# Kernel optimization log

Hardware: AMD Instinct MI355X
Metric: run time of the kernel (lower is better)

Reference implementation:

```python
import jax, jax.numpy as jnp
import numpy as np

B, L, E, H = 2, 1024, 1024, 16
D = E // H  # head_dim = 64
EPS = 1e-6


def setup_inputs() -> dict:
    key = jax.random.key(0)
    ks = jax.random.split(key, 6)
    x = jax.random.normal(ks[0], (B, L, E), dtype=jnp.float32)
    qkv_w = jax.random.normal(ks[1], (E, 3 * E), dtype=jnp.float32) / np.sqrt(E)
    qkv_b = jnp.zeros((3 * E,), dtype=jnp.float32)
    out_w = jax.random.normal(ks[2], (E, E), dtype=jnp.float32) / np.sqrt(E)
    out_b = jnp.zeros((E,), dtype=jnp.float32)
    norm1_w = jnp.ones((E,), dtype=jnp.float32)
    norm2_w = jnp.ones((E,), dtype=jnp.float32)
    mlp_w1 = jax.random.normal(ks[3], (E, 4 * E), dtype=jnp.float32) / np.sqrt(E)
    mlp_b1 = jnp.zeros((4 * E,), dtype=jnp.float32)
    mlp_w2 = jax.random.normal(ks[4], (4 * E, E), dtype=jnp.float32) / np.sqrt(4 * E)
    mlp_b2 = jnp.zeros((E,), dtype=jnp.float32)
    return dict(x=x, qkv_w=qkv_w, qkv_b=qkv_b, out_w=out_w, out_b=out_b,
                norm1_w=norm1_w, norm2_w=norm2_w,
                mlp_w1=mlp_w1, mlp_b1=mlp_b1, mlp_w2=mlp_w2, mlp_b2=mlp_b2)


def rmsnorm(x, w, eps=1e-6):
    var = jnp.mean(jnp.square(x), axis=-1, keepdims=True)
    return x * jax.lax.rsqrt(var + eps) * w


def cosformer_attn(x, qkv_w, qkv_b, out_w, out_b):
    b, l, e = x.shape
    qkv = x @ qkv_w + qkv_b
    q, k, v = jnp.split(qkv, 3, axis=-1)
    # [B, H, L, D]
    q = q.reshape(b, l, H, D).transpose(0, 2, 1, 3)
    k = k.reshape(b, l, H, D).transpose(0, 2, 1, 3)
    v = v.reshape(b, l, H, D).transpose(0, 2, 1, 3)
    positions = jnp.arange(l, dtype=jnp.float32).reshape(1, 1, l, 1)
    cos_w = jnp.cos(jnp.pi / 2 * positions / l)
    sin_w = jnp.sin(jnp.pi / 2 * positions / l)
    q_prime = jax.nn.relu(q)
    k_prime = jax.nn.relu(k)
    q_cos, q_sin = q_prime * cos_w, q_prime * sin_w
    k_cos, k_sin = k_prime * cos_w, k_prime * sin_w
    # running KV state: cumsum over L of per-position outer products [B,H,L,D,D]
    kv_cos_cumsum = jnp.cumsum(jnp.einsum('bhld,bhle->bhlde', k_cos, v), axis=2)
    context_cos = jnp.einsum('bhld,bhlde->bhle', q_cos, kv_cos_cumsum)
    kv_sin_cumsum = jnp.cumsum(jnp.einsum('bhld,bhle->bhlde', k_sin, v), axis=2)
    context_sin = jnp.einsum('bhld,bhlde->bhle', q_sin, kv_sin_cumsum)
    context = context_cos + context_sin
    k_cos_cumsum = jnp.cumsum(k_cos, axis=2)
    k_sin_cumsum = jnp.cumsum(k_sin, axis=2)
    norm = (jnp.einsum('bhld,bhld->bhl', q_cos, k_cos_cumsum)
            + jnp.einsum('bhld,bhld->bhl', q_sin, k_sin_cumsum))
    output = context / (norm[..., None] + EPS)
    output = output.transpose(0, 2, 1, 3).reshape(b, l, e)
    return output @ out_w + out_b


def reference(x, qkv_w, qkv_b, out_w, out_b, norm1_w, norm2_w,
              mlp_w1, mlp_b1, mlp_w2, mlp_b2):
    # pre-norm transformer block with cosformer causal linear attention
    h = x + cosformer_attn(rmsnorm(x, norm1_w), qkv_w, qkv_b, out_w, out_b)
    m = rmsnorm(h, norm2_w)
    m = jax.nn.gelu(m @ mlp_w1 + mlp_b1) @ mlp_w2 + mlp_b2
    return h + m
```

## Files before the change

kernel.cpp:

```cpp
#include <hip/hip_runtime.h>

#define TB_L 1024
#define TB_E 1024

typedef __attribute__((ext_vector_type(8))) short bf16x8;
typedef __attribute__((ext_vector_type(8))) unsigned short u16x8;
typedef __attribute__((ext_vector_type(4))) float floatx4;

#define AS1(p) ((const __attribute__((address_space(1))) void*)(p))
#define AS3(p) ((__attribute__((address_space(3))) void*)(p))

static __device__ __forceinline__ unsigned short f2bf(float x) {
  union { float f; unsigned u; } c; c.f = x;
  unsigned r = c.u + 0x7fff + ((c.u >> 16) & 1);
  return (unsigned short)(r >> 16);
}
static __device__ __forceinline__ float gelu_f(float x) {
  const float c0 = 0.7978845608028654f;
  const float c1 = 0.044715f;
  float x3 = x * x * x;
  return 0.5f * x * (1.0f + tanhf(c0 * (x + c1 * x3)));
}

static __device__ __forceinline__ int swz(int row, int bytecol) {
  return row * 128 +
         ((((bytecol >> 4) ^ ((row + (row >> 3)) & 7)) << 4) | (bytecol & 15));
}

__global__ __launch_bounds__(256) void rms_kernel(const float* __restrict__ x,
                                                  const float* __restrict__ w,
                                                  unsigned short* __restrict__ out) {
  const int row = blockIdx.x;
  const int tid = threadIdx.x;
  const float4 v = *(const float4*)(x + (size_t)row * TB_E + tid * 4);
  float s = v.x * v.x + v.y * v.y + v.z * v.z + v.w * v.w;
#pragma unroll
  for (int off = 32; off > 0; off >>= 1) s += __shfl_down(s, off);
  __shared__ float red[4];
  if ((tid & 63) == 0) red[tid >> 6] = s;
  __syncthreads();
  const float tot = red[0] + red[1] + red[2] + red[3];
  const float scale = rsqrtf(tot * (1.0f / TB_E) + 1e-6f);
  const float4 wv = *(const float4*)(w + tid * 4);
  ushort4 o;
  o.x = f2bf(v.x * scale * wv.x);
  o.y = f2bf(v.y * scale * wv.y);
  o.z = f2bf(v.z * scale * wv.z);
  o.w = f2bf(v.w * scale * wv.w);
  *(ushort4*)(out + (size_t)row * TB_E + tid * 4) = o;
}

__global__ __launch_bounds__(256) void transpose_all(
    const float* __restrict__ s0, const float* __restrict__ s1,
    const float* __restrict__ s2, const float* __restrict__ s3,
    unsigned short* __restrict__ d0, unsigned short* __restrict__ d1,
    unsigned short* __restrict__ d2, unsigned short* __restrict__ d3) {
  const int id = blockIdx.x;
  const float* in; unsigned short* out; int K, N, lid;
  if (id < 768)       { in = s0; out = d0; K = 1024; N = 3072; lid = id; }
  else if (id < 1024) { in = s1; out = d1; K = 1024; N = 1024; lid = id - 768; }
  else if (id < 2048) { in = s2; out = d2; K = 1024; N = 4096; lid = id - 1024; }
  else                { in = s3; out = d3; K = 4096; N = 1024; lid = id - 2048; }
  const int nx = N >> 6;
  const int n0 = (lid % nx) * 64, k0 = (lid / nx) * 64;
  __shared__ float t[64][65];
  const int tid = threadIdx.x;
#pragma unroll
  for (int rep = 0; rep < 4; ++rep) {
    const int r = rep * 16 + (tid >> 4);
    const int c = (tid & 15) * 4;
    const float4 v = *(const float4*)(in + (size_t)(k0 + r) * N + n0 + c);
    t[r][c] = v.x; t[r][c + 1] = v.y; t[r][c + 2] = v.z; t[r][c + 3] = v.w;
  }
  __syncthreads();
#pragma unroll
  for (int rep = 0; rep < 4; ++rep) {
    const int n = rep * 16 + (tid >> 4);
    const int k = (tid & 15) * 4;
    ushort4 o;
    o.x = f2bf(t[k + 0][n]);
    o.y = f2bf(t[k + 1][n]);
    o.z = f2bf(t[k + 2][n]);
    o.w = f2bf(t[k + 3][n]);
    *(ushort4*)(out + (size_t)(n0 + n) * K + k0 + k) = o;
  }
}

template <int BM, int BN, int BK, int WM, int WN, int NTH, bool GELU>
__global__ __launch_bounds__(NTH) void gemm_bf16(
    const unsigned short* __restrict__ A, const unsigned short* __restrict__ Bt,
    const float* __restrict__ bias, const float* __restrict__ res,
    float* __restrict__ Cf, unsigned short* __restrict__ Cb,
    float* __restrict__ Cpart, int M, int N, int K, int Ksl) {
  constexpr int NW = NTH / 64;
  constexpr int KC = BK / 32;
  constexpr int WCOLS = BN / WN;
  constexpr int MT = WM / 16;
  constexpr int NT = WN / 16;
  constexpr int ACH = (BM / 16) * KC;
  constexpr int BCH = (BN / 16) * KC;
  static_assert((BM / WM) * (BN / WN) == NW, "wave grid");
  static_assert(ACH % NW == 0 && BCH % NW == 0, "chunks divisible by waves");
  __shared__ __align__(16) unsigned short As[2][BM * BK];
  __shared__ __align__(16) unsigned short Bs[2][BN * BK];
  const int tid = threadIdx.x;
  const int wid = tid >> 6, lane = tid & 63;

  constexpr int G = 4;
  const int nbx = gridDim.x;
  const int flat = blockIdx.y * nbx + blockIdx.x;
  const int grp = flat / (G * nbx), rem = flat % (G * nbx);
  const int m0 = (grp * G + rem % G) * BM;
  const int n0 = (rem / G) * BN;

  const int k_off = blockIdx.z * Ksl;
  const int mbase = (wid / WCOLS) * WM, nbase = (wid % WCOLS) * WN;

  floatx4 acc[MT][NT];
#pragma unroll
  for (int i = 0; i < MT; ++i)
#pragma unroll
    for (int j = 0; j < NT; ++j) {
      floatx4 z = {0.f, 0.f, 0.f, 0.f};
      acc[i][j] = z;
    }

  const int srow = lane >> 2;
  const int scol = (lane & 3) * 8;
  const unsigned short* Ag = A + (size_t)m0 * K + k_off;
  const unsigned short* Bg = Bt + (size_t)n0 * K + k_off;
  const int fr = (lane & 15);
  const int fk = (lane >> 4) * 16;

  auto stage = [&](int buf, int k0) {
#pragma unroll
    for (int j = 0; j < ACH / NW; ++j) {
      const int ch = j * NW + wid;
      const int strip = ch / KC, half = ch % KC;
      __builtin_amdgcn_global_load_lds(
          AS1(Ag + (size_t)(strip * 16 + srow) * K + k0 + half * 32 + scol),
          AS3((char*)&As[buf][0] + ch * 1024), 16, 0, 0);
    }
#pragma unroll
    for (int j = 0; j < BCH / NW; ++j) {
      const int ch = j * NW + wid;
      const int strip = ch / KC, half = ch % KC;
      __builtin_amdgcn_global_load_lds(
          AS1(Bg + (size_t)(strip * 16 + srow) * K + k0 + half * 32 + scol),
          AS3((char*)&Bs[buf][0] + ch * 1024), 16, 0, 0);
    }
  };

  stage(0, 0);
  const int nsteps = Ksl / BK;
  for (int s = 0; s < nsteps; ++s) {
    __syncthreads();
    const int cur = s & 1;
    if (s + 1 < nsteps) stage(cur ^ 1, (s + 1) * BK);
    const char* Ab = (const char*)&As[cur][0];
    const char* Bb = (const char*)&Bs[cur][0];
#pragma unroll
    for (int g = 0; g < KC; ++g) {
      bf16x8 af[MT], bfr[NT];
#pragma unroll
      for (int i = 0; i < MT; ++i)
        af[i] = *(const bf16x8*)(Ab + ((mbase / 16 + i) * KC + g) * 1024 +
                                 fr * 64 + fk);
#pragma unroll
      for (int j = 0; j < NT; ++j)
        bfr[j] = *(const bf16x8*)(Bb + ((nbase / 16 + j) * KC + g) * 1024 +
                                  fr * 64 + fk);
#pragma unroll
      for (int i = 0; i < MT; ++i)
#pragma unroll
        for (int j = 0; j < NT; ++j)
          acc[i][j] = __builtin_amdgcn_mfma_f32_16x16x32_bf16(af[i], bfr[j],
                                                              acc[i][j], 0, 0, 0);
    }
  }

  const int mr = (lane >> 4) * 4;
  const int nc = lane & 15;
  float* P = Cpart ? (Cpart + (size_t)blockIdx.z * M * N) : nullptr;
#pragma unroll
  for (int i = 0; i < MT; ++i)
#pragma unroll
    for (int j = 0; j < NT; ++j) {
      const int n = n0 + nbase + j * 16 + nc;
      const float bv = bias ? bias[n] : 0.f;
#pragma unroll
      for (int r = 0; r < 4; ++r) {
        const int m = m0 + mbase + i * 16 + mr + r;
        float v = acc[i][j][r] + bv;
        if (GELU) v = gelu_f(v);
        if (res) v += res[(size_t)m * N + n];
        if (P) P[(size_t)m * N + n] = v;
        if (Cf) Cf[(size_t)m * N + n] = v;
        if (Cb) Cb[(size_t)m * N + n] = f2bf(v);
      }
    }
}

__global__ __launch_bounds__(256) void reduce_out(const float* __restrict__ P,
                                                  const float* __restrict__ h,
                                                  const float* __restrict__ b2,
                                                  float* __restrict__ out) {
  const int idx = (blockIdx.x * 256 + threadIdx.x) * 4;
  const int n = idx & 1023;
  const float4 a = *(const float4*)(P + idx);
  const float4 b = *(const float4*)(P + 2097152 + idx);
  const float4 hh = *(const float4*)(h + idx);
  const float4 bb = *(const float4*)(b2 + n);
  float4 o;
  o.x = a.x + b.x + hh.x + bb.x;
  o.y = a.y + b.y + hh.y + bb.y;
  o.z = a.z + b.z + hh.z + bb.z;
  o.w = a.w + b.w + hh.w + bb.w;
  *(float4*)(out + idx) = o;
}

__global__ __launch_bounds__(256) void attn_mfma(const unsigned short* __restrict__ qkv,
                                                 unsigned short* __restrict__ out) {
  const int it = blockIdx.x;
  const int bh = blockIdx.y;
  const int b = bh >> 4, h = bh & 15;
  const int tid = threadIdx.x;
  const int w = tid >> 6, lane = tid & 63;
  const int qd = lane >> 4, ln = lane & 15;
  const int i0 = it * 64;
  __shared__ __align__(16) char sq[8192];
  __shared__ __align__(16) char sk[8192];
  __shared__ __align__(16) char svt[8192];
  __shared__ __align__(16) char ss[8192];
  const unsigned short* base = qkv + (size_t)b * (TB_L * 3072) + h * 64;
  const float PH = 1.5339807878856412e-3f;

#pragma unroll
  for (int p = 0; p < 2; ++p) {
    const int flat = p * 256 + tid;
    const int r = flat >> 3, c = flat & 7;
    u16x8 v = *(const u16x8*)(base + (size_t)(i0 + r) * 3072 + c * 8);
#pragma unroll
    for (int z = 0; z < 8; ++z) v[z] = (v[z] & 0x8000) ? (unsigned short)0 : v[z];
    *(u16x8*)(sq + swz(r, c * 16)) = v;
  }
  __syncthreads();

  bf16x8 aq[2];
#pragma unroll
  for (int ks = 0; ks < 2; ++ks)
    aq[ks] = *(const bf16x8*)(sq + swz(w * 16 + ln, ks * 64 + qd * 16));

  float ci[4], si[4];
#pragma unroll
  for (int r = 0; r < 4; ++r)
    __sincosf(PH * (float)(i0 + w * 16 + qd * 4 + r), &si[r], &ci[r]);

  floatx4 acc_o[4], acc_n;
  {
    floatx4 z = {0.f, 0.f, 0.f, 0.f};
#pragma unroll
    for (int nt = 0; nt < 4; ++nt) acc_o[nt] = z;
    acc_n = z;
  }
  bf16x8 ones;
#pragma unroll
  for (int z = 0; z < 8; ++z) ones[z] = (short)0x3F80;

  for (int jt = 0; jt <= it; ++jt) {
    const int j0 = jt * 64;
    __syncthreads();
#pragma unroll
    for (int p = 0; p < 2; ++p) {
      const int flat = p * 256 + tid;
      const int r = flat >> 3, c = flat & 7;
      u16x8 kv = *(const u16x8*)(base + (size_t)(j0 + r) * 3072 + 1024 + c * 8);
#pragma unroll
      for (int z = 0; z < 8; ++z) kv[z] = (kv[z] & 0x8000) ? (unsigned short)0 : kv[z];
      *(u16x8*)(sk + swz(r, c * 16)) = kv;
      u16x8 vv = *(const u16x8*)(base + (size_t)(j0 + r) * 3072 + 2048 + c * 8);
#pragma unroll
      for (int z = 0; z < 8; ++z)
        *(unsigned short*)(svt + swz(c * 8 + z, r * 2)) = (unsigned short)vv[z];
    }
    __syncthreads();

    floatx4 s_acc[4];
    {
      floatx4 z = {0.f, 0.f, 0.f, 0.f};
#pragma unroll
      for (int nt = 0; nt < 4; ++nt) s_acc[nt] = z;
    }
#pragma unroll
    for (int ks = 0; ks < 2; ++ks)
#pragma unroll
      for (int nt = 0; nt < 4; ++nt) {
        const bf16x8 bk = *(const bf16x8*)(sk + swz(nt * 16 + ln, ks * 64 + qd * 16));
        s_acc[nt] = __builtin_amdgcn_mfma_f32_16x16x32_bf16(aq[ks], bk, s_acc[nt], 0, 0, 0);
      }

    float cj[4], sj[4];
#pragma unroll
    for (int nt = 0; nt < 4; ++nt)
      __sincosf(PH * (float)(j0 + nt * 16 + ln), &sj[nt], &cj[nt]);
    const bool diag = (jt == it);
    const int li = w * 16 + qd * 4;
#pragma unroll
    for (int nt = 0; nt < 4; ++nt) {
      const int jl = nt * 16 + ln;
#pragma unroll
      for (int r = 0; r < 4; ++r) {
        float val = s_acc[nt][r] * (ci[r] * cj[nt] + si[r] * sj[nt]);
        if (diag && jl > li + r) val = 0.f;
        *(unsigned short*)(ss + swz(li + r, jl * 2)) = f2bf(val);
      }
    }

#pragma unroll
    for (int ks = 0; ks < 2; ++ks) {
      const bf16x8 as = *(const bf16x8*)(ss + swz(w * 16 + ln, ks * 64 + qd * 16));
#pragma unroll
      for (int nt = 0; nt < 4; ++nt) {
        const bf16x8 bv = *(const bf16x8*)(svt + swz(nt * 16 + ln, ks * 64 + qd * 16));
        acc_o[nt] = __builtin_amdgcn_mfma_f32_16x16x32_bf16(as, bv, acc_o[nt], 0, 0, 0);
      }
      acc_n = __builtin_amdgcn_mfma_f32_16x16x32_bf16(as, ones, acc_n, 0, 0, 0);
    }
  }

#pragma unroll
  for (int r = 0; r < 4; ++r) {
    const float inv = 1.0f / (acc_n[r] + 1e-6f);
    unsigned short* op =
        out + (size_t)(b * TB_L + i0 + w * 16 + qd * 4 + r) * TB_E + h * 64;
#pragma unroll
    for (int nt = 0; nt < 4; ++nt) op[nt * 16 + ln] = f2bf(acc_o[nt][r] * inv);
  }
}

extern "C" void kernel_launch(void* const* d_in, const int* in_sizes, int n_in,
                              void* d_out, int out_size, void* d_ws, size_t ws_size,
                              hipStream_t stream) {
  const float* x     = (const float*)d_in[0];
  const float* qkv_w = (const float*)d_in[1];
  const float* qkv_b = (const float*)d_in[2];
  const float* out_w = (const float*)d_in[3];
  const float* out_b = (const float*)d_in[4];
  const float* n1w   = (const float*)d_in[5];
  const float* n2w   = (const float*)d_in[6];
  const float* w1    = (const float*)d_in[7];
  const float* b1    = (const float*)d_in[8];
  const float* w2    = (const float*)d_in[9];
  const float* b2    = (const float*)d_in[10];

  char* wsb = (char*)d_ws;
  unsigned short* qkvb  = (unsigned short*)wsb;
  unsigned short* g     = (unsigned short*)wsb;
  unsigned short* xnb   = (unsigned short*)(wsb + 16777216);
  unsigned short* attnb = (unsigned short*)(wsb + 20971520);
  float*          h     = (float*)(wsb + 25165824);
  unsigned short* qkvwt = (unsigned short*)(wsb + 33554432);
  unsigned short* outwt = (unsigned short*)(wsb + 39845888);
  unsigned short* w1t   = (unsigned short*)(wsb + 41943040);
  unsigned short* w2t   = (unsigned short*)(wsb + 50331648);
  float*          Pk    = (float*)(wsb + 33554432);
  float* out = (float*)d_out;
  const int M = 2048;

  transpose_all<<<dim3(3072), 256, 0, stream>>>(qkv_w, out_w, w1, w2,
                                                qkvwt, outwt, w1t, w2t);

  rms_kernel<<<dim3(M), 256, 0, stream>>>(x, n1w, xnb);
  gemm_bf16<64, 128, 64, 32, 32, 512, false><<<dim3(24, 32), 512, 0, stream>>>(
      xnb, qkvwt, qkv_b, nullptr, nullptr, qkvb, nullptr, M, 3072, 1024, 1024);
  attn_mfma<<<dim3(16, 32), 256, 0, stream>>>(qkvb, attnb);
  gemm_bf16<64, 64, 64, 32, 32, 256, false><<<dim3(16, 32), 256, 0, stream>>>(
      attnb, outwt, out_b, x, h, nullptr, nullptr, M, 1024, 1024, 1024);
  rms_kernel<<<dim3(M), 256, 0, stream>>>(h, n2w, xnb);
  gemm_bf16<64, 128, 64, 32, 32, 512, true><<<dim3(32, 32), 512, 0, stream>>>(
      xnb, w1t, b1, nullptr, nullptr, g, nullptr, M, 4096, 1024, 1024);
  gemm_bf16<64, 128, 64, 32, 32, 512, false><<<dim3(8, 32, 2), 512, 0, stream>>>(
      g, w2t, nullptr, nullptr, nullptr, nullptr, Pk, M, 1024, 4096, 2048);
  reduce_out<<<dim3(2048), 256, 0, stream>>>(Pk, h, b2, out);
}
```

Baseline: 264.8 us.

## Fuse ReLU and V-transpose into QKV GEMM, double-buffer attention K/V via direct LDS loads

The QKV GEMM epilogue now applies ReLU to the Q and K columns and also writes V pre-transposed per head into a separate workspace buffer. The attention kernel therefore no longer masks signs or transposes V in registers. It loads Q, K and V^T straight into LDS with global_load_lds, double-buffers the K/V tiles so the next tile is fetched during compute, and uses a simpler swizzle. The grid is reordered to (bh, it) so blocks sharing a head run together. In exchange, the GEMM epilogue writes extra data, and the new swizzle and direct-LDS layout must agree exactly with the fragment reads.

```diff
diff --git a/kernel.cpp b/kernel.cpp
--- a/kernel.cpp
+++ b/kernel.cpp
@@ -23,8 +23,7 @@
 }
 
 static __device__ __forceinline__ int swz(int row, int bytecol) {
-  return row * 128 +
-         ((((bytecol >> 4) ^ ((row + (row >> 3)) & 7)) << 4) | (bytecol & 15));
+  return row * 128 + ((((bytecol >> 4) ^ (row & 7)) << 4) | (bytecol & 15));
 }
 
 __global__ __launch_bounds__(256) void rms_kernel(const float* __restrict__ x,
@@ -86,12 +85,13 @@
   }
 }
 
-template <int BM, int BN, int BK, int WM, int WN, int NTH, bool GELU>
+template <int BM, int BN, int BK, int WM, int WN, int NTH, bool GELU, bool VT>
 __global__ __launch_bounds__(NTH) void gemm_bf16(
     const unsigned short* __restrict__ A, const unsigned short* __restrict__ Bt,
     const float* __restrict__ bias, const float* __restrict__ res,
     float* __restrict__ Cf, unsigned short* __restrict__ Cb,
-    float* __restrict__ Cpart, int M, int N, int K, int Ksl) {
+    float* __restrict__ Cpart, unsigned short* __restrict__ vtp,
+    int relu_ncut, int M, int N, int K, int Ksl) {
   constexpr int NW = NTH / 64;
   constexpr int KC = BK / 32;
   constexpr int WCOLS = BN / WN;
@@ -188,15 +188,27 @@
     for (int j = 0; j < NT; ++j) {
       const int n = n0 + nbase + j * 16 + nc;
       const float bv = bias ? bias[n] : 0.f;
+      float tv[4];
 #pragma unroll
       for (int r = 0; r < 4; ++r) {
         const int m = m0 + mbase + i * 16 + mr + r;
         float v = acc[i][j][r] + bv;
         if (GELU) v = gelu_f(v);
+        if (n < relu_ncut) v = fmaxf(v, 0.f);
         if (res) v += res[(size_t)m * N + n];
         if (P) P[(size_t)m * N + n] = v;
         if (Cf) Cf[(size_t)m * N + n] = v;
         if (Cb) Cb[(size_t)m * N + n] = f2bf(v);
+        tv[r] = v;
+      }
+      if (VT && n >= 2048) {
+        const int mm = m0 + mbase + i * 16 + mr;
+        const int bb = mm >> 10, l = mm & 1023;
+        const int hh = (n - 2048) >> 6, dd = (n - 2048) & 63;
+        ushort4 o;
+        o.x = f2bf(tv[0]); o.y = f2bf(tv[1]);
+        o.z = f2bf(tv[2]); o.w = f2bf(tv[3]);
+        *(ushort4*)(vtp + (size_t)(bb * 16 + hh) * 65536 + dd * 1024 + l) = o;
       }
     }
 }
@@ -219,31 +231,53 @@
   *(float4*)(out + idx) = o;
 }
 
-__global__ __launch_bounds__(256) void attn_mfma(const unsigned short* __restrict__ qkv,
-                                                 unsigned short* __restrict__ out) {
-  const int it = blockIdx.x;
-  const int bh = blockIdx.y;
+__global__ __launch_bounds__(256) void attn_mfma(
+    const unsigned short* __restrict__ qkv,
+    const unsigned short* __restrict__ vt,
+    unsigned short* __restrict__ out) {
+  const int bh = blockIdx.x;
+  const int it = blockIdx.y;
   const int b = bh >> 4, h = bh & 15;
   const int tid = threadIdx.x;
   const int w = tid >> 6, lane = tid & 63;
   const int qd = lane >> 4, ln = lane & 15;
   const int i0 = it * 64;
   __shared__ __align__(16) char sq[8192];
-  __shared__ __align__(16) char sk[8192];
-  __shared__ __align__(16) char svt[8192];
+  __shared__ __align__(16) char sk[2][8192];
+  __shared__ __align__(16) char sv[2][8192];
   __shared__ __align__(16) char ss[8192];
-  const unsigned short* base = qkv + (size_t)b * (TB_L * 3072) + h * 64;
+  const unsigned short* qbase = qkv + (size_t)b * (TB_L * 3072) + h * 64;
+  const unsigned short* kbase = qbase + 1024;
+  const unsigned short* vbase = vt + (size_t)bh * 65536;
   const float PH = 1.5339807878856412e-3f;
 
+  const int sr = lane >> 3;
+  const int cg = ((lane & 7) ^ sr) * 8;
+
 #pragma unroll
   for (int p = 0; p < 2; ++p) {
-    const int flat = p * 256 + tid;
-    const int r = flat >> 3, c = flat & 7;
-    u16x8 v = *(const u16x8*)(base + (size_t)(i0 + r) * 3072 + c * 8);
-#pragma unroll
-    for (int z = 0; z < 8; ++z) v[z] = (v[z] & 0x8000) ? (unsigned short)0 : v[z];
-    *(u16x8*)(sq + swz(r, c * 16)) = v;
-  }
+    const int ch = p * 4 + w;
+    __builtin_amdgcn_global_load_lds(
+        AS1(qbase + (size_t)(i0 + ch * 8 + sr) * 3072 + cg),
+        AS3(sq + ch * 1024), 16, 0, 0);
+  }
+  auto stage_kv = [&](int buf, int jt) {
+    const int j0 = jt * 64;
+#pragma unroll
+    for (int p = 0; p < 4; ++p) {
+      const int ch = p * 4 + w;
+      if (ch < 8) {
+        __builtin_amdgcn_global_load_lds(
+            AS1(kbase + (size_t)(j0 + ch * 8 + sr) * 3072 + cg),
+            AS3(sk[buf] + ch * 1024), 16, 0, 0);
+      } else {
+        __builtin_amdgcn_global_load_lds(
+            AS1(vbase + (size_t)((ch - 8) * 8 + sr) * 1024 + j0 + cg),
+            AS3(sv[buf] + (ch - 8) * 1024), 16, 0, 0);
+      }
+    }
+  };
+  stage_kv(0, 0);
   __syncthreads();
 
   bf16x8 aq[2];
@@ -268,22 +302,11 @@
   for (int z = 0; z < 8; ++z) ones[z] = (short)0x3F80;
 
   for (int jt = 0; jt <= it; ++jt) {
+    const int cur = jt & 1;
+    if (jt < it) stage_kv(cur ^ 1, jt + 1);
+    const char* skb = sk[cur];
+    const char* svb = sv[cur];
     const int j0 = jt * 64;
-    __syncthreads();
-#pragma unroll
-    for (int p = 0; p < 2; ++p) {
-      const int flat = p * 256 + tid;
-      const int r = flat >> 3, c = flat & 7;
-      u16x8 kv = *(const u16x8*)(base + (size_t)(j0 + r) * 3072 + 1024 + c * 8);
-#pragma unroll
-      for (int z = 0; z < 8; ++z) kv[z] = (kv[z] & 0x8000) ? (unsigned short)0 : kv[z];
-      *(u16x8*)(sk + swz(r, c * 16)) = kv;
-      u16x8 vv = *(const u16x8*)(base + (size_t)(j0 + r) * 3072 + 2048 + c * 8);
-#pragma unroll
-      for (int z = 0; z < 8; ++z)
-        *(unsigned short*)(svt + swz(c * 8 + z, r * 2)) = (unsigned short)vv[z];
-    }
-    __syncthreads();
 
     floatx4 s_acc[4];
     {
@@ -295,8 +318,10 @@
     for (int ks = 0; ks < 2; ++ks)
 #pragma unroll
       for (int nt = 0; nt < 4; ++nt) {
-        const bf16x8 bk = *(const bf16x8*)(sk + swz(nt * 16 + ln, ks * 64 + qd * 16));
-        s_acc[nt] = __builtin_amdgcn_mfma_f32_16x16x32_bf16(aq[ks], bk, s_acc[nt], 0, 0, 0);
+        const bf16x8 bk =
+            *(const bf16x8*)(skb + swz(nt * 16 + ln, ks * 64 + qd * 16));
+        s_acc[nt] =
+            __builtin_amdgcn_mfma_f32_16x16x32_bf16(aq[ks], bk, s_acc[nt], 0, 0, 0);
       }
 
     float cj[4], sj[4];
@@ -321,11 +346,14 @@
       const bf16x8 as = *(const bf16x8*)(ss + swz(w * 16 + ln, ks * 64 + qd * 16));
 #pragma unroll
       for (int nt = 0; nt < 4; ++nt) {
-        const bf16x8 bv = *(const bf16x8*)(svt + swz(nt * 16 + ln, ks * 64 + qd * 16));
-        acc_o[nt] = __builtin_amdgcn_mfma_f32_16x16x32_bf16(as, bv, acc_o[nt], 0, 0, 0);
+        const bf16x8 bv =
+            *(const bf16x8*)(svb + swz(nt * 16 + ln, ks * 64 + qd * 16));
+        acc_o[nt] =
+            __builtin_amdgcn_mfma_f32_16x16x32_bf16(as, bv, acc_o[nt], 0, 0, 0);
       }
       acc_n = __builtin_amdgcn_mfma_f32_16x16x32_bf16(as, ones, acc_n, 0, 0, 0);
     }
+    __syncthreads();
   }
 
 #pragma unroll
@@ -356,6 +384,7 @@
   char* wsb = (char*)d_ws;
   unsigned short* qkvb  = (unsigned short*)wsb;
   unsigned short* g     = (unsigned short*)wsb;
+  unsigned short* vt    = (unsigned short*)(wsb + 12582912);
   unsigned short* xnb   = (unsigned short*)(wsb + 16777216);
   unsigned short* attnb = (unsigned short*)(wsb + 20971520);
   float*          h     = (float*)(wsb + 25165824);
@@ -371,15 +400,15 @@
                                                 qkvwt, outwt, w1t, w2t);
 
   rms_kernel<<<dim3(M), 256, 0, stream>>>(x, n1w, xnb);
-  gemm_bf16<64, 128, 64, 32, 32, 512, false><<<dim3(24, 32), 512, 0, stream>>>(
-      xnb, qkvwt, qkv_b, nullptr, nullptr, qkvb, nullptr, M, 3072, 1024, 1024);
-  attn_mfma<<<dim3(16, 32), 256, 0, stream>>>(qkvb, attnb);
-  gemm_bf16<64, 64, 64, 32, 32, 256, false><<<dim3(16, 32), 256, 0, stream>>>(
-      attnb, outwt, out_b, x, h, nullptr, nullptr, M, 1024, 1024, 1024);
+  gemm_bf16<64, 128, 64, 32, 32, 512, false, true><<<dim3(24, 32), 512, 0, stream>>>(
+      xnb, qkvwt, qkv_b, nullptr, nullptr, qkvb, nullptr, vt, 2048, M, 3072, 1024, 1024);
+  attn_mfma<<<dim3(32, 16), 256, 0, stream>>>(qkvb, vt, attnb);
+  gemm_bf16<64, 64, 64, 32, 32, 256, false, false><<<dim3(16, 32), 256, 0, stream>>>(
+      attnb, outwt, out_b, x, h, nullptr, nullptr, nullptr, 0, M, 1024, 1024, 1024);
   rms_kernel<<<dim3(M), 256, 0, stream>>>(h, n2w, xnb);
-  gemm_bf16<64, 128, 64, 32, 32, 512, true><<<dim3(32, 32), 512, 0, stream>>>(
-      xnb, w1t, b1, nullptr, nullptr, g, nullptr, M, 4096, 1024, 1024);
-  gemm_bf16<64, 128, 64, 32, 32, 512, false><<<dim3(8, 32, 2), 512, 0, stream>>>(
-      g, w2t, nullptr, nullptr, nullptr, nullptr, Pk, M, 1024, 4096, 2048);
+  gemm_bf16<64, 128, 64, 32, 32, 512, true, false><<<dim3(32, 32), 512, 0, stream>>>(
+      xnb, w1t, b1, nullptr, nullptr, g, nullptr, nullptr, 0, M, 4096, 1024, 1024);
+  gemm_bf16<64, 128, 64, 32, 32, 512, false, false><<<dim3(8, 32, 2), 512, 0, stream>>>(
+      g, w2t, nullptr, nullptr, nullptr, nullptr, Pk, nullptr, 0, M, 1024, 4096, 2048);
   reduce_out<<<dim3(2048), 256, 0, stream>>>(Pk, h, b2, out);
 }
```

Result: faster. 248.4 us (-6.2%).
